# Optimization experiments

Measured on AMD Instinct MI355X. Metric: run time of the kernel, lower is better.

## Reference

```python
import jax, jax.numpy as jnp
import numpy as np

B, S, HID, NH, INTER = 1, 2048, 1024, 16, 4096
D = INTER // NH  # per-head intermediate dim = 256


def setup_inputs() -> dict:
    key = jax.random.key(0)
    ks = jax.random.split(key, 10)
    w = lambda k, shp: jax.random.normal(k, shp, jnp.float32) * 0.02
    return {
        "x": jax.random.normal(ks[0], (B, S, HID), jnp.float32),
        "adjacency": jax.random.uniform(ks[1], (B, NH, S, S), jnp.float32),
        "Wg": w(ks[2], (INTER, HID)),   # gate_proj.weight (out,in)
        "Wu": w(ks[3], (INTER, HID)),   # up_proj.weight
        "Wd": w(ks[4], (HID, INTER)),   # down_proj.weight
        "eps": jnp.zeros((NH,), jnp.float32),   # GIN epsilons (init 0)
        "alpha": jnp.ones((NH,), jnp.float32),  # sum-agg scales (init 1)
        "Wq": w(ks[5], (NH, D, D)),     # per-head attn_query_projs weights (out,in)
        "Wk": w(ks[6], (NH, D, D)),     # per-head attn_key_projs weights
        "W1": w(ks[7], (D, 4 * D)),     # aggregator_mlp[0].weight
        "W2": w(ks[8], (D, D)),         # aggregator_mlp[2].weight
    }


def reference(x, adjacency, Wg, Wu, Wd, eps, alpha, Wq, Wk, W1, W2):
    b, s, _ = x.shape
    nh, d, _ = Wq.shape
    # first half of SwiGLU MLP
    h = jax.nn.silu(x @ Wg.T) * (x @ Wu.T)            # (b, s, inter)
    h = h.reshape(b, s, nh, d).transpose(0, 2, 1, 3)  # (b, h, s, d)
    # GIN original term
    orig = (1.0 + eps)[None, :, None, None] * h
    # sum aggregation over adjacency
    sum_agg = alpha[None, :, None, None] * jnp.einsum('bhij,bhjd->bhid', adjacency, h)
    # max over identical expanded copies of h along the neighbor axis == h itself
    max_agg = h
    # adjacency-log-masked attention aggregation
    Q = jnp.einsum('bhsd,hed->bhse', h, Wq)
    K = jnp.einsum('bhsd,hed->bhse', h, Wk)
    scores = jnp.einsum('bhse,bhte->bhst', Q, K) / jnp.sqrt(jnp.float32(d))
    scores = scores + jnp.log(adjacency + 1e-9)
    attn = jax.nn.softmax(scores, axis=-1)
    attn_agg = jnp.einsum('bhst,bhtd->bhsd', attn, h)
    # 4-way concat + aggregator MLP (per head, shared weights)
    comb = jnp.concatenate([orig, sum_agg, max_agg, attn_agg], axis=-1)  # (b,h,s,4d)
    gin = jnp.einsum('bhsd,od->bhso', jax.nn.silu(jnp.einsum('bhsi,oi->bhso', comb, W1)), W2)
    # recombine heads and finish MLP
    gin = gin.transpose(0, 2, 1, 3).reshape(b, s, nh * d)
    return gin @ Wd.T
```

## Files before the change

kernel.cpp:

```cpp
#include <hip/hip_runtime.h>

typedef unsigned short u16;
typedef __attribute__((ext_vector_type(4))) float f32x4;
typedef __attribute__((ext_vector_type(8))) short s16x8;
typedef __attribute__((ext_vector_type(4))) short s16x4;

#define DEVI static __device__ __forceinline__

constexpr int S = 2048, HID = 1024, NH = 16, D = 256, INTER = 4096;

constexpr size_t N_XB   = (size_t)S*HID;
constexpr size_t N_W    = (size_t)INTER*HID;
constexpr size_t N_WQK  = (size_t)NH*D*D;
constexpr size_t N_W1C  = (size_t)NH*D*768;
constexpr size_t N_W2   = (size_t)D*D;
constexpr size_t N_COMB = (size_t)NH*S*768;
constexpr size_t N_HB   = (size_t)NH*S*D;

constexpr size_t O_XB   = 0;
constexpr size_t O_WG   = O_XB + N_XB;
constexpr size_t O_WU   = O_WG + N_W;
constexpr size_t O_WD   = O_WU + N_W;
constexpr size_t O_WQ   = O_WD + N_W;
constexpr size_t O_WK   = O_WQ + N_WQK;
constexpr size_t O_W1C  = O_WK + N_WQK;
constexpr size_t O_W2   = O_W1C + N_W1C;
constexpr size_t O_COMB = O_W2 + N_W2;
constexpr size_t O_HB   = O_COMB + N_COMB;
constexpr size_t O_QB   = O_HB + N_HB;
constexpr size_t O_KC   = O_QB + N_HB;

DEVI u16 f2bf(float f) {
  union { float f; unsigned u; } v; v.f = f;
  unsigned r = v.u + 0x7FFFu + ((v.u >> 16) & 1u);
  return (u16)(r >> 16);
}

DEVI float bf2f(u16 b) {
  union { unsigned u; float f; } v; v.u = ((unsigned)b) << 16;
  return v.f;
}

DEVI void gload16(const void* g, const void* l) {
  __builtin_amdgcn_global_load_lds(
      (const __attribute__((address_space(1))) unsigned int*)g,
      (__attribute__((address_space(3))) unsigned int*)l, 16, 0, 0);
}

DEVI f32x4 ntload(const float* p) {
  return __builtin_nontemporal_load((const f32x4*)p);
}

DEVI void stage_rm(const u16* src, int stride, u16* lds, int tid) {
  const int wid = tid >> 6;
#pragma unroll
  for (int i = 0; i < 2; ++i) {
    int c = i * 256 + tid;
    gload16(src + (size_t)(c & 127) * stride + (c >> 7) * 8,
            lds + (size_t)(i * 256 + wid * 64) * 8);
  }
}

DEVI void stage_rm64(const u16* src, int stride, u16* lds, int tid) {
  const int wid = tid >> 6;
  gload16(src + (size_t)(tid & 63) * stride + (tid >> 6) * 8,
          lds + (size_t)(wid * 64) * 8);
}

DEVI s16x8 ldfrag(const u16* lds, int kp, int row) {
  return *(const s16x8*)(lds + ((size_t)kp * 128 + row) * 8);
}

DEVI s16x8 ldfrag64(const u16* lds, int kp, int row) {
  return *(const s16x8*)(lds + ((size_t)kp * 64 + row) * 8);
}

__global__ void k_convert(const float* __restrict__ x,  const float* __restrict__ Wg,
                          const float* __restrict__ Wu, const float* __restrict__ Wd,
                          const float* __restrict__ Wq, const float* __restrict__ Wk,
                          const float* __restrict__ W1, const float* __restrict__ W2,
                          const float* __restrict__ eps, const float* __restrict__ alpha,
                          u16* __restrict__ ws) {
  const size_t totv = (N_XB + 3 * N_W + 2 * N_WQK) / 4;
  for (size_t vi = (size_t)blockIdx.x * blockDim.x + threadIdx.x; vi < totv;
       vi += (size_t)gridDim.x * blockDim.x) {
    size_t j = vi * 4;
    const float* src; size_t dst;
    if (j < N_XB)                { src = x  + j;                    dst = O_XB + j; }
    else if ((j -= N_XB) < N_W)  { src = Wg + j;                    dst = O_WG + j; }
    else if ((j -= N_W) < N_W)   { src = Wu + j;                    dst = O_WU + j; }
    else if ((j -= N_W) < N_W)   { src = Wd + j;                    dst = O_WD + j; }
    else if ((j -= N_W) < N_WQK) { src = Wq + j;                    dst = O_WQ + j; }
    else   { j -= N_WQK;           src = Wk + j;                    dst = O_WK + j; }
    f32x4 v = *(const f32x4*)src;
    s16x4 w;
    w[0] = (short)f2bf(v[0]); w[1] = (short)f2bf(v[1]);
    w[2] = (short)f2bf(v[2]); w[3] = (short)f2bf(v[3]);
    *(s16x4*)(ws + dst) = w;
  }
  const size_t tot2 = N_W2 + N_W1C;
  for (size_t i = (size_t)blockIdx.x * blockDim.x + threadIdx.x; i < tot2;
       i += (size_t)gridDim.x * blockDim.x) {
    size_t j = i;
    if (j < N_W2) { ws[O_W2 + j] = f2bf(W2[(j % D) * D + (j / D)]); continue; } j -= N_W2;
    size_t h = j / ((size_t)D * 768);
    size_t r = j % ((size_t)D * 768);
    size_t o = r / 768, c = r % 768;
    float v;
    if (c < 256)      v = (1.f + eps[h]) * W1[o * 1024 + c] + W1[o * 1024 + 512 + c];
    else if (c < 512) v = alpha[h] * W1[o * 1024 + c];
    else              v = W1[o * 1024 + 256 + c];
    ws[O_W1C + j] = f2bf(v);
  }
}

template <int MODE>
__global__ __launch_bounds__(256, 2) void k_dual(const u16* __restrict__ Ab,
                                                 const u16* __restrict__ B0b,
                                                 const u16* __restrict__ B1b,
                                                 u16* __restrict__ o0, u16* __restrict__ o1) {
  __shared__ u16 lA[4096], lB0[4096], lB1[4096];
  const int tid = threadIdx.x, lane = tid & 63, wid = tid >> 6;
  const int wm = wid >> 1, wn = wid & 1;
  const int m0 = blockIdx.x * 128, nt = blockIdx.y, head = blockIdx.z;

  const int K  = (MODE == 0) ? HID : D;
  const int sA = (MODE == 0) ? HID : 768;
  const int sB = (MODE == 0) ? HID : D;
  const u16* A  = (MODE == 0) ? (Ab + (size_t)m0 * HID)
                              : (Ab + ((size_t)head * S + m0) * 768);
  const u16* B0 = (MODE == 0) ? (B0b + (size_t)nt * 128 * HID)
                              : (B0b + (size_t)head * D * D + (size_t)nt * 128 * D);
  const u16* B1 = (MODE == 0) ? (B1b + (size_t)nt * 128 * HID)
                              : (B1b + (size_t)head * D * D + (size_t)nt * 128 * D);

  f32x4 a0[4][4], a1[4][4];
#pragma unroll
  for (int i = 0; i < 4; ++i)
#pragma unroll
    for (int j = 0; j < 4; ++j) { a0[i][j] = f32x4{0.f,0.f,0.f,0.f}; a1[i][j] = f32x4{0.f,0.f,0.f,0.f}; }

  for (int k0 = 0; k0 < K; k0 += 32) {
    __syncthreads();
    stage_rm(A  + k0, sA, lA,  tid);
    stage_rm(B0 + k0, sB, lB0, tid);
    stage_rm(B1 + k0, sB, lB1, tid);
    __syncthreads();
    const int kp = lane >> 4, r = lane & 15;
    s16x8 af[4], b0f[4], b1f[4];
#pragma unroll
    for (int f = 0; f < 4; ++f) {
      af[f]  = ldfrag(lA,  kp, wm * 64 + f * 16 + r);
      b0f[f] = ldfrag(lB0, kp, wn * 64 + f * 16 + r);
      b1f[f] = ldfrag(lB1, kp, wn * 64 + f * 16 + r);
    }
#pragma unroll
    for (int fi = 0; fi < 4; ++fi)
#pragma unroll
      for (int fj = 0; fj < 4; ++fj) {
        a0[fi][fj] = __builtin_amdgcn_mfma_f32_16x16x32_bf16(af[fi], b0f[fj], a0[fi][fj], 0, 0, 0);
        a1[fi][fj] = __builtin_amdgcn_mfma_f32_16x16x32_bf16(af[fi], b1f[fj], a1[fi][fj], 0, 0, 0);
      }
  }

#pragma unroll
  for (int fi = 0; fi < 4; ++fi)
#pragma unroll
    for (int fj = 0; fj < 4; ++fj)
#pragma unroll
      for (int reg = 0; reg < 4; ++reg) {
        int row = m0 + wm * 64 + fi * 16 + ((lane >> 4) * 4 + reg);
        int cl  = wn * 64 + fj * 16 + (lane & 15);
        if (MODE == 0) {
          int col = nt * 128 + cl;
          float g = a0[fi][fj][reg], uu = a1[fi][fj][reg];
          float h = g / (1.f + __expf(-g)) * uu;
          u16 hb = f2bf(h);
          int hh = col >> 8, d = col & 255;
          o0[((size_t)hh * S + row) * 768 + d] = hb;
          o1[(((size_t)hh * (S / 8) + (row >> 3)) * 256 + d) * 8 + (row & 7)] = hb;
        } else {
          int e = nt * 128 + cl;
          o0[((size_t)head * S + row) * D + e] = f2bf(a0[fi][fj][reg]);
          o1[(((size_t)head * 32 + (e >> 3)) * S + row) * 8 + (e & 7)] = f2bf(a1[fi][fj][reg]);
        }
      }
}

__global__ __launch_bounds__(256, 2) void k_attn(const float* __restrict__ adj,
                                                 const u16* __restrict__ Qb,
                                                 const u16* __restrict__ Kc,
                                                 const u16* __restrict__ hB,
                                                 u16* __restrict__ comb) {
  __shared__ u16 lK[2][1024 * 8];
  __shared__ u16 lH[2][1024 * 8];
  __shared__ u16 lAdj[2][64 * 36];
  __shared__ u16 lP[4][16 * 36];
  const int tid = threadIdx.x, lane = tid & 63, wid = tid >> 6;
  const int bid  = blockIdx.x;
  const int slot = bid & 7;
  const int idx  = bid >> 3;
  const int head = slot + 8 * (idx >> 5);
  const int bx   = idx & 31;
  const int q0 = bx * 64 + wid * 16;
  const int l15 = lane & 15, l4 = lane >> 4;

  s16x8 q[8];
  {
    const u16* qr = Qb + ((size_t)head * S + q0 + l15) * D + l4 * 8;
#pragma unroll
    for (int ks = 0; ks < 8; ++ks) q[ks] = *(const s16x8*)(qr + ks * 32);
  }
  f32x4 accO[16], accS[16];
#pragma unroll
  for (int i = 0; i < 16; ++i) { accO[i] = f32x4{0.f,0.f,0.f,0.f}; accS[i] = f32x4{0.f,0.f,0.f,0.f}; }
  float m_r[4] = {-1e30f, -1e30f, -1e30f, -1e30f};
  float l_r[4] = {0.f, 0.f, 0.f, 0.f};

  const float* adjB = adj + ((size_t)head * S + bx * 64) * S;
  const int arow = tid >> 3;
  const int acol = (tid & 7) * 4;

#pragma unroll
  for (int i = 0; i < 4; ++i) {
    int c = i * 256 + tid;
    gload16(Kc + ((size_t)(head * 32 + (c >> 5)) * S + (c & 31)) * 8,
            &lK[0][(size_t)(i * 256 + wid * 64) * 8]);
  }
#pragma unroll
  for (int i = 0; i < 4; ++i) {
    int c = i * 256 + tid;
    gload16(hB + ((size_t)(head * (S / 8) + (c >> 8)) * 256 + (c & 255)) * 8,
            &lH[0][(size_t)(i * 256 + wid * 64) * 8]);
  }
  f32x4 av0 = ntload(adjB + (size_t)arow * S + acol);
  f32x4 av1 = ntload(adjB + (size_t)(arow + 32) * S + acol);

  auto TILE = [&](int t0, int cur) {
    const int t1 = (t0 + 32 < S) ? t0 + 32 : t0;
#pragma unroll
    for (int i = 0; i < 4; ++i) {
      int c = i * 256 + tid;
      gload16(Kc + ((size_t)(head * 32 + (c >> 5)) * S + t1 + (c & 31)) * 8,
              &lK[cur ^ 1][(size_t)(i * 256 + wid * 64) * 8]);
    }
#pragma unroll
    for (int i = 0; i < 4; ++i) {
      int c = i * 256 + tid;
      gload16(hB + ((size_t)(head * (S / 8) + (t1 >> 3) + (c >> 8)) * 256 + (c & 255)) * 8,
              &lH[cur ^ 1][(size_t)(i * 256 + wid * 64) * 8]);
    }
    f32x4 nv0 = ntload(adjB + (size_t)arow * S + t1 + acol);
    f32x4 nv1 = ntload(adjB + (size_t)(arow + 32) * S + t1 + acol);
    {
      s16x4 w;
      w[0] = (short)f2bf(av0[0]); w[1] = (short)f2bf(av0[1]);
      w[2] = (short)f2bf(av0[2]); w[3] = (short)f2bf(av0[3]);
      *(s16x4*)(&lAdj[cur][(size_t)arow * 36 + acol]) = w;
      w[0] = (short)f2bf(av1[0]); w[1] = (short)f2bf(av1[1]);
      w[2] = (short)f2bf(av1[2]); w[3] = (short)f2bf(av1[3]);
      *(s16x4*)(&lAdj[cur][(size_t)(arow + 32) * 36 + acol]) = w;
    }
    asm volatile("s_waitcnt vmcnt(10) lgkmcnt(0)" ::: "memory");
    __builtin_amdgcn_s_barrier();
    __builtin_amdgcn_sched_barrier(0);

    const u16* lKc = &lK[cur][0];
    const u16* lHc = &lH[cur][0];
    const u16* lAc = &lAdj[cur][0];

    f32x4 scA[2], scB[2];
    scA[0] = f32x4{0.f,0.f,0.f,0.f}; scA[1] = f32x4{0.f,0.f,0.f,0.f};
    scB[0] = f32x4{0.f,0.f,0.f,0.f}; scB[1] = f32x4{0.f,0.f,0.f,0.f};
#pragma unroll
    for (int ks = 0; ks < 4; ++ks)
#pragma unroll
      for (int fj = 0; fj < 2; ++fj) {
        s16x8 b0 = *(const s16x8*)(lKc + ((size_t)(ks * 4 + l4) * 32 + fj * 16 + l15) * 8);
        s16x8 b1 = *(const s16x8*)(lKc + ((size_t)((ks + 4) * 4 + l4) * 32 + fj * 16 + l15) * 8);
        scA[fj] = __builtin_amdgcn_mfma_f32_16x16x32_bf16(q[ks], b0, scA[fj], 0, 0, 0);
        scB[fj] = __builtin_amdgcn_mfma_f32_16x16x32_bf16(q[ks + 4], b1, scB[fj], 0, 0, 0);
      }

    float av[2][4];
#pragma unroll
    for (int fj = 0; fj < 2; ++fj)
#pragma unroll
      for (int reg = 0; reg < 4; ++reg)
        av[fj][reg] = bf2f(lAc[(size_t)(wid * 16 + l4 * 4 + reg) * 36 + fj * 16 + l15]);

    float sf[2][4];
#pragma unroll
    for (int fj = 0; fj < 2; ++fj)
#pragma unroll
      for (int reg = 0; reg < 4; ++reg)
        sf[fj][reg] = (scA[fj][reg] + scB[fj][reg]) * 0.0625f;

    bool chg = false;
    float lmax[4];
#pragma unroll
    for (int reg = 0; reg < 4; ++reg) {
      lmax[reg] = fmaxf(sf[0][reg], sf[1][reg]);
      chg |= (lmax[reg] > m_r[reg] + 8.f);
    }
    if (__any((int)chg)) {
      float scl[4];
#pragma unroll
      for (int reg = 0; reg < 4; ++reg) {
        float m = lmax[reg];
#pragma unroll
        for (int off = 1; off < 16; off <<= 1) m = fmaxf(m, __shfl_xor(m, off));
        float mn = fmaxf(m_r[reg], m);
        scl[reg] = __expf(m_r[reg] - mn);
        m_r[reg] = mn;
        l_r[reg] *= scl[reg];
      }
#pragma unroll
      for (int nf = 0; nf < 16; ++nf) {
        f32x4 t = accO[nf];
        t[0] *= scl[0]; t[1] *= scl[1]; t[2] *= scl[2]; t[3] *= scl[3];
        accO[nf] = t;
      }
    }
    u16 pb[2][4];
#pragma unroll
    for (int fj = 0; fj < 2; ++fj)
#pragma unroll
      for (int reg = 0; reg < 4; ++reg) {
        float p = (av[fj][reg] + 1e-9f) * exp2f((sf[fj][reg] - m_r[reg]) * 1.44269504f);
        l_r[reg] += p;
        pb[fj][reg] = f2bf(p);
      }

    u16* pl = &lP[wid][0];
#pragma unroll
    for (int fj = 0; fj < 2; ++fj)
#pragma unroll
      for (int reg = 0; reg < 4; ++reg)
        pl[(size_t)(l4 * 4 + reg) * 36 + fj * 16 + l15] = pb[fj][reg];
    asm volatile("s_waitcnt lgkmcnt(0)" ::: "memory");
    __builtin_amdgcn_sched_barrier(0);

    s16x8 pa, aa;
    {
      s16x4 plo = *(const s16x4*)(pl + (size_t)l15 * 36 + l4 * 8);
      s16x4 phi = *(const s16x4*)(pl + (size_t)l15 * 36 + l4 * 8 + 4);
      pa[0] = plo[0]; pa[1] = plo[1]; pa[2] = plo[2]; pa[3] = plo[3];
      pa[4] = phi[0]; pa[5] = phi[1]; pa[6] = phi[2]; pa[7] = phi[3];
      s16x4 alo = *(const s16x4*)(lAc + (size_t)(wid * 16 + l15) * 36 + l4 * 8);
      s16x4 ahi = *(const s16x4*)(lAc + (size_t)(wid * 16 + l15) * 36 + l4 * 8 + 4);
      aa[0] = alo[0]; aa[1] = alo[1]; aa[2] = alo[2]; aa[3] = alo[3];
      aa[4] = ahi[0]; aa[5] = ahi[1]; aa[6] = ahi[2]; aa[7] = ahi[3];
    }
#pragma unroll
    for (int nf = 0; nf < 16; ++nf) {
      s16x8 hb = *(const s16x8*)(lHc + ((size_t)l4 * 256 + nf * 16 + l15) * 8);
      accO[nf] = __builtin_amdgcn_mfma_f32_16x16x32_bf16(pa, hb, accO[nf], 0, 0, 0);
      accS[nf] = __builtin_amdgcn_mfma_f32_16x16x32_bf16(aa, hb, accS[nf], 0, 0, 0);
    }

    av0 = nv0; av1 = nv1;

    __builtin_amdgcn_sched_barrier(0);
    __builtin_amdgcn_s_barrier();
  };

  for (int t0 = 0; t0 < S; t0 += 64) {
    TILE(t0, 0);
    TILE(t0 + 32, 1);
  }

  asm volatile("s_waitcnt vmcnt(0)" ::: "memory");

#pragma unroll
  for (int reg = 0; reg < 4; ++reg) {
#pragma unroll
    for (int off = 1; off < 16; off <<= 1) l_r[reg] += __shfl_xor(l_r[reg], off);
  }
  float inv[4];
#pragma unroll
  for (int reg = 0; reg < 4; ++reg) inv[reg] = 1.f / l_r[reg];
#pragma unroll
  for (int nf = 0; nf < 16; ++nf)
#pragma unroll
    for (int reg = 0; reg < 4; ++reg) {
      size_t rb = ((size_t)head * S + q0 + l4 * 4 + reg) * 768;
      comb[rb + 512 + nf * 16 + l15] = f2bf(accO[nf][reg] * inv[reg]);
      comb[rb + 256 + nf * 16 + l15] = f2bf(accS[nf][reg]);
    }
}

template <int MODE>
__global__ __launch_bounds__(256, 2) void k_gemm(const u16* __restrict__ Ab,
                                                 const u16* __restrict__ Bb,
                                                 u16* __restrict__ oU, float* __restrict__ oF) {
  constexpr int BN = (MODE == 2) ? 64 : 128;
  constexpr int FJ = BN / 32;
  __shared__ u16 lA[4096], lB[BN * 32];
  const int tid = threadIdx.x, lane = tid & 63, wid = tid >> 6;
  const int wm = wid >> 1, wn = wid & 1;
  const int m0 = blockIdx.x * 128, nt = blockIdx.y, head = blockIdx.z;

  constexpr int K  = (MODE == 0) ? 768 : (MODE == 2) ? INTER : D;
  constexpr int sA = (MODE == 3) ? INTER : K;
  constexpr int sB = K;
  const u16* A = (MODE == 0) ? Ab + ((size_t)head * S + m0) * 768
               : (MODE == 2) ? Ab + (size_t)m0 * INTER
                             : Ab + (size_t)m0 * INTER + head * D;
  const u16* B = (MODE == 0) ? Bb + ((size_t)head * D + nt * 128) * 768
                             : Bb + (size_t)nt * BN * sB;

  f32x4 acc[4][FJ];
#pragma unroll
  for (int i = 0; i < 4; ++i)
#pragma unroll
    for (int j = 0; j < FJ; ++j) acc[i][j] = f32x4{0.f,0.f,0.f,0.f};

  for (int k0 = 0; k0 < K; k0 += 32) {
    __syncthreads();
    stage_rm(A + k0, sA, lA, tid);
    if constexpr (BN == 128) stage_rm(B + k0, sB, lB, tid);
    else                     stage_rm64(B + k0, sB, lB, tid);
    __syncthreads();
    const int kp = lane >> 4, r = lane & 15;
    s16x8 af[4], bf[FJ];
#pragma unroll
    for (int f = 0; f < 4; ++f) af[f] = ldfrag(lA, kp, wm * 64 + f * 16 + r);
#pragma unroll
    for (int f = 0; f < FJ; ++f) {
      if constexpr (BN == 128) bf[f] = ldfrag(lB, kp, wn * 64 + f * 16 + r);
      else                     bf[f] = ldfrag64(lB, kp, wn * 32 + f * 16 + r);
    }
#pragma unroll
    for (int fi = 0; fi < 4; ++fi)
#pragma unroll
      for (int fj = 0; fj < FJ; ++fj)
        acc[fi][fj] = __builtin_amdgcn_mfma_f32_16x16x32_bf16(af[fi], bf[fj], acc[fi][fj], 0, 0, 0);
  }

#pragma unroll
  for (int fi = 0; fi < 4; ++fi)
#pragma unroll
    for (int fj = 0; fj < FJ; ++fj)
#pragma unroll
      for (int reg = 0; reg < 4; ++reg) {
        int row = m0 + wm * 64 + fi * 16 + ((lane >> 4) * 4 + reg);
        int cn = nt * BN + wn * (BN / 2) + fj * 16 + (lane & 15);
        float v = acc[fi][fj][reg];
        if (MODE == 0) {
          v = v / (1.f + __expf(-v));
          oU[(size_t)row * INTER + head * D + cn] = f2bf(v);
        } else if (MODE == 3) {
          oU[(size_t)row * INTER + head * D + cn] = f2bf(v);
        } else {
          oF[(size_t)row * HID + cn] = v;
        }
      }
}

extern "C" void kernel_launch(void* const* d_in, const int* in_sizes, int n_in,
                              void* d_out, int out_size, void* d_ws, size_t ws_size,
                              hipStream_t stream) {
  const float* x     = (const float*)d_in[0];
  const float* adj   = (const float*)d_in[1];
  const float* Wg    = (const float*)d_in[2];
  const float* Wu    = (const float*)d_in[3];
  const float* Wd    = (const float*)d_in[4];
  const float* eps   = (const float*)d_in[5];
  const float* alpha = (const float*)d_in[6];
  const float* Wq    = (const float*)d_in[7];
  const float* Wk    = (const float*)d_in[8];
  const float* W1    = (const float*)d_in[9];
  const float* W2    = (const float*)d_in[10];
  u16* ws = (u16*)d_ws;

  k_convert<<<dim3(4096), dim3(256), 0, stream>>>(x, Wg, Wu, Wd, Wq, Wk, W1, W2, eps, alpha, ws);
  k_dual<0><<<dim3(16, 32, 1), dim3(256), 0, stream>>>(ws + O_XB, ws + O_WG, ws + O_WU,
                                                       ws + O_COMB, ws + O_HB);
  k_dual<1><<<dim3(16, 2, 16), dim3(256), 0, stream>>>(ws + O_COMB, ws + O_WQ, ws + O_WK,
                                                       ws + O_QB, ws + O_KC);
  k_attn<<<dim3(512), dim3(256), 0, stream>>>(adj, ws + O_QB, ws + O_KC, ws + O_HB, ws + O_COMB);
  k_gemm<3><<<dim3(8, 2, 16), dim3(256), 0, stream>>>(ws + O_WD, ws + O_W2, ws + O_KC, nullptr);
  k_gemm<0><<<dim3(16, 2, 16), dim3(256), 0, stream>>>(ws + O_COMB, ws + O_W1C, ws + O_QB, nullptr);
  k_gemm<2><<<dim3(16, 16, 1), dim3(256), 0, stream>>>(ws + O_QB, ws + O_KC, nullptr, (float*)d_out);
}
```

Baseline: 385.0 us.

## Single-buffer attention LDS tiles to raise occupancy to three blocks per CU

Replaces the double-buffered K, H and adjacency LDS tiles in the attention kernel with single buffers. K and H loads are now staggered: the next K tile is issued right after the QK MFMAs, and the next H tile after the PV MFMAs, with extra barriers and vmcnt waits between them. Launch bounds rise from 2 to 3 blocks per CU, using the smaller LDS footprint to hide latency through occupancy instead of intra-block prefetch. The cost is two more block barriers per tile, less overlap inside each block, and register pressure under the tighter launch bound that may cause spills.

```diff
diff --git a/kernel.cpp b/kernel.cpp
--- a/kernel.cpp
+++ b/kernel.cpp
@@ -187,14 +187,14 @@
       }
 }
 
-__global__ __launch_bounds__(256, 2) void k_attn(const float* __restrict__ adj,
+__global__ __launch_bounds__(256, 3) void k_attn(const float* __restrict__ adj,
                                                  const u16* __restrict__ Qb,
                                                  const u16* __restrict__ Kc,
                                                  const u16* __restrict__ hB,
                                                  u16* __restrict__ comb) {
-  __shared__ u16 lK[2][1024 * 8];
-  __shared__ u16 lH[2][1024 * 8];
-  __shared__ u16 lAdj[2][64 * 36];
+  __shared__ u16 lK[1024 * 8];
+  __shared__ u16 lH[1024 * 8];
+  __shared__ u16 lAdj[64 * 36];
   __shared__ u16 lP[4][16 * 36];
   const int tid = threadIdx.x, lane = tid & 63, wid = tid >> 6;
   const int bid  = blockIdx.x;
@@ -221,53 +221,44 @@
   const int arow = tid >> 3;
   const int acol = (tid & 7) * 4;
 
-#pragma unroll
-  for (int i = 0; i < 4; ++i) {
-    int c = i * 256 + tid;
-    gload16(Kc + ((size_t)(head * 32 + (c >> 5)) * S + (c & 31)) * 8,
-            &lK[0][(size_t)(i * 256 + wid * 64) * 8]);
-  }
-#pragma unroll
-  for (int i = 0; i < 4; ++i) {
-    int c = i * 256 + tid;
-    gload16(hB + ((size_t)(head * (S / 8) + (c >> 8)) * 256 + (c & 255)) * 8,
-            &lH[0][(size_t)(i * 256 + wid * 64) * 8]);
-  }
+  auto issueK = [&](int t) {
+#pragma unroll
+    for (int i = 0; i < 4; ++i) {
+      int c = i * 256 + tid;
+      gload16(Kc + ((size_t)(head * 32 + (c >> 5)) * S + t + (c & 31)) * 8,
+              lK + (size_t)(i * 256 + wid * 64) * 8);
+    }
+  };
+  auto issueH = [&](int t) {
+#pragma unroll
+    for (int i = 0; i < 4; ++i) {
+      int c = i * 256 + tid;
+      gload16(hB + ((size_t)(head * (S / 8) + (t >> 3) + (c >> 8)) * 256 + (c & 255)) * 8,
+              lH + (size_t)(i * 256 + wid * 64) * 8);
+    }
+  };
+
+  issueK(0);
   f32x4 av0 = ntload(adjB + (size_t)arow * S + acol);
   f32x4 av1 = ntload(adjB + (size_t)(arow + 32) * S + acol);
-
-  auto TILE = [&](int t0, int cur) {
+  issueH(0);
+
+  for (int t0 = 0; t0 < S; t0 += 32) {
     const int t1 = (t0 + 32 < S) ? t0 + 32 : t0;
-#pragma unroll
-    for (int i = 0; i < 4; ++i) {
-      int c = i * 256 + tid;
-      gload16(Kc + ((size_t)(head * 32 + (c >> 5)) * S + t1 + (c & 31)) * 8,
-              &lK[cur ^ 1][(size_t)(i * 256 + wid * 64) * 8]);
-    }
-#pragma unroll
-    for (int i = 0; i < 4; ++i) {
-      int c = i * 256 + tid;
-      gload16(hB + ((size_t)(head * (S / 8) + (t1 >> 3) + (c >> 8)) * 256 + (c & 255)) * 8,
-              &lH[cur ^ 1][(size_t)(i * 256 + wid * 64) * 8]);
-    }
-    f32x4 nv0 = ntload(adjB + (size_t)arow * S + t1 + acol);
-    f32x4 nv1 = ntload(adjB + (size_t)(arow + 32) * S + t1 + acol);
+
+    asm volatile("s_waitcnt vmcnt(4)" ::: "memory");
     {
       s16x4 w;
       w[0] = (short)f2bf(av0[0]); w[1] = (short)f2bf(av0[1]);
       w[2] = (short)f2bf(av0[2]); w[3] = (short)f2bf(av0[3]);
-      *(s16x4*)(&lAdj[cur][(size_t)arow * 36 + acol]) = w;
+      *(s16x4*)(lAdj + (size_t)arow * 36 + acol) = w;
       w[0] = (short)f2bf(av1[0]); w[1] = (short)f2bf(av1[1]);
       w[2] = (short)f2bf(av1[2]); w[3] = (short)f2bf(av1[3]);
-      *(s16x4*)(&lAdj[cur][(size_t)(arow + 32) * 36 + acol]) = w;
-    }
-    asm volatile("s_waitcnt vmcnt(10) lgkmcnt(0)" ::: "memory");
+      *(s16x4*)(lAdj + (size_t)(arow + 32) * 36 + acol) = w;
+    }
+    asm volatile("s_waitcnt lgkmcnt(0)" ::: "memory");
     __builtin_amdgcn_s_barrier();
     __builtin_amdgcn_sched_barrier(0);
-
-    const u16* lKc = &lK[cur][0];
-    const u16* lHc = &lH[cur][0];
-    const u16* lAc = &lAdj[cur][0];
 
     f32x4 scA[2], scB[2];
     scA[0] = f32x4{0.f,0.f,0.f,0.f}; scA[1] = f32x4{0.f,0.f,0.f,0.f};
@@ -276,18 +267,23 @@
     for (int ks = 0; ks < 4; ++ks)
 #pragma unroll
       for (int fj = 0; fj < 2; ++fj) {
-        s16x8 b0 = *(const s16x8*)(lKc + ((size_t)(ks * 4 + l4) * 32 + fj * 16 + l15) * 8);
-        s16x8 b1 = *(const s16x8*)(lKc + ((size_t)((ks + 4) * 4 + l4) * 32 + fj * 16 + l15) * 8);
+        s16x8 b0 = *(const s16x8*)(lK + ((size_t)(ks * 4 + l4) * 32 + fj * 16 + l15) * 8);
+        s16x8 b1 = *(const s16x8*)(lK + ((size_t)((ks + 4) * 4 + l4) * 32 + fj * 16 + l15) * 8);
         scA[fj] = __builtin_amdgcn_mfma_f32_16x16x32_bf16(q[ks], b0, scA[fj], 0, 0, 0);
         scB[fj] = __builtin_amdgcn_mfma_f32_16x16x32_bf16(q[ks + 4], b1, scB[fj], 0, 0, 0);
       }
+    __builtin_amdgcn_s_barrier();
+    __builtin_amdgcn_sched_barrier(0);
+    issueK(t1);
+    f32x4 nv0 = ntload(adjB + (size_t)arow * S + t1 + acol);
+    f32x4 nv1 = ntload(adjB + (size_t)(arow + 32) * S + t1 + acol);
 
     float av[2][4];
 #pragma unroll
     for (int fj = 0; fj < 2; ++fj)
 #pragma unroll
       for (int reg = 0; reg < 4; ++reg)
-        av[fj][reg] = bf2f(lAc[(size_t)(wid * 16 + l4 * 4 + reg) * 36 + fj * 16 + l15]);
+        av[fj][reg] = bf2f(lAdj[(size_t)(wid * 16 + l4 * 4 + reg) * 36 + fj * 16 + l15]);
 
     float sf[2][4];
 #pragma unroll
@@ -347,27 +343,28 @@
       s16x4 phi = *(const s16x4*)(pl + (size_t)l15 * 36 + l4 * 8 + 4);
       pa[0] = plo[0]; pa[1] = plo[1]; pa[2] = plo[2]; pa[3] = plo[3];
       pa[4] = phi[0]; pa[5] = phi[1]; pa[6] = phi[2]; pa[7] = phi[3];
-      s16x4 alo = *(const s16x4*)(lAc + (size_t)(wid * 16 + l15) * 36 + l4 * 8);
-      s16x4 ahi = *(const s16x4*)(lAc + (size_t)(wid * 16 + l15) * 36 + l4 * 8 + 4);
+      s16x4 alo = *(const s16x4*)(lAdj + (size_t)(wid * 16 + l15) * 36 + l4 * 8);
+      s16x4 ahi = *(const s16x4*)(lAdj + (size_t)(wid * 16 + l15) * 36 + l4 * 8 + 4);
       aa[0] = alo[0]; aa[1] = alo[1]; aa[2] = alo[2]; aa[3] = alo[3];
       aa[4] = ahi[0]; aa[5] = ahi[1]; aa[6] = ahi[2]; aa[7] = ahi[3];
     }
+
+    asm volatile("s_waitcnt vmcnt(6)" ::: "memory");
+    __builtin_amdgcn_s_barrier();
+    __builtin_amdgcn_sched_barrier(0);
+
 #pragma unroll
     for (int nf = 0; nf < 16; ++nf) {
-      s16x8 hb = *(const s16x8*)(lHc + ((size_t)l4 * 256 + nf * 16 + l15) * 8);
+      s16x8 hb = *(const s16x8*)(lH + ((size_t)l4 * 256 + nf * 16 + l15) * 8);
       accO[nf] = __builtin_amdgcn_mfma_f32_16x16x32_bf16(pa, hb, accO[nf], 0, 0, 0);
       accS[nf] = __builtin_amdgcn_mfma_f32_16x16x32_bf16(aa, hb, accS[nf], 0, 0, 0);
     }
 
     av0 = nv0; av1 = nv1;
 
+    __builtin_amdgcn_s_barrier();
     __builtin_amdgcn_sched_barrier(0);
-    __builtin_amdgcn_s_barrier();
-  };
-
-  for (int t0 = 0; t0 < S; t0 += 64) {
-    TILE(t0, 0);
-    TILE(t0 + 32, 1);
+    issueH(t1);
   }
 
   asm volatile("s_waitcnt vmcnt(0)" ::: "memory");
```

After: 921.2 us. 2.39x slower.
